# Kernel optimization log

Hardware: AMD Instinct MI355X
Metric: run time of the kernel (lower is better)

The kernel has to match this reference:

```python
import jax, jax.numpy as jnp
import numpy as np

B, T, C, H, M, MEM_FREQ = 1, 2048, 768, 12, 64, 64


def setup_inputs() -> dict:
    key = jax.random.key(0)
    k1, k2, k3 = jax.random.split(key, 3)
    x = jax.random.normal(k1, (B, T, C), jnp.float32)
    # landmark ('mem') token every MEM_FREQ positions, as in landmark-attention data prep
    is_mem = jnp.broadcast_to((jnp.arange(T) % MEM_FREQ == MEM_FREQ - 1)[None, :], (B, T))
    w_qkv = 0.02 * jax.random.normal(k2, (C, 3 * C), jnp.float32)
    b_qkv = jnp.zeros((3 * C,), jnp.float32)
    w_proj = 0.02 * jax.random.normal(k3, (C, C), jnp.float32)
    b_proj = jnp.zeros((C,), jnp.float32)
    return {"x": x, "is_mem": is_mem, "w_qkv": w_qkv, "b_qkv": b_qkv,
            "w_proj": w_proj, "b_proj": b_proj}


def _grouped_softmax(att, im, mask, last_sec):
    """LandmarkGroupedSoftmaxFunction + landmark_grouped_softmax (eval, no dropout).
    att/im/mask/last_sec: (B,H,T,T); softmax over last dim grouped into M buckets."""
    neg = -jnp.inf
    last_and_rest = last_sec | mask
    full_access = im | last_and_rest
    mem_group_idx = jnp.cumsum(im.astype(jnp.int32), axis=-1)  # (B,H,T,T)
    resp = jnp.where(last_and_rest | im, M - 1, mem_group_idx)  # bucket id per key

    R = att.shape[0] * att.shape[1] * att.shape[2]
    Tk = att.shape[3]
    xf = att.reshape(R, Tk)
    idxf = resp.reshape(R, Tk)

    row_max = jax.vmap(lambda xr, ir: jnp.full((M,), neg, xr.dtype).at[ir].max(xr))
    row_sum = jax.vmap(lambda xr, ir: jnp.zeros((M,), xr.dtype).at[ir].add(xr))

    max_by_group = row_max(xf, idxf)                                   # (R,M)
    maxes = jnp.take_along_axis(max_by_group, idxf, axis=-1)
    safe_max = jnp.where(jnp.isinf(maxes), 0.0, maxes)
    x_exp = jnp.exp(xf - safe_max)
    denom_g = row_sum(x_exp, idxf)
    denom = jnp.take_along_axis(denom_g, idxf, axis=-1)
    small = denom < 0.5
    probs = jnp.where(small, 0.0, x_exp / jnp.where(small, 1.0, denom))

    imf = im.reshape(R, Tk)
    lsf = last_sec.reshape(R, Tk)
    faf = full_access.reshape(R, Tk)
    # group_prob[g] = prob of landmark g; last slot = mass of last (current) section
    gp_idx = jnp.where(imf, mem_group_idx.reshape(R, Tk) - 1, M - 1)
    group_prob = row_sum(jnp.where(imf, probs, 0.0), gp_idx)
    group_prob = group_prob.at[:, M - 1].set(jnp.sum(probs * lsf, axis=-1))
    gathered = jnp.take_along_axis(group_prob, idxf, axis=-1)
    mult = jnp.where(faf, lsf.astype(probs.dtype), gathered)
    return (probs * mult).reshape(att.shape)


def reference(x, is_mem, w_qkv, b_qkv, w_proj, b_proj):
    Bx, Tx, Cx = x.shape
    hd = Cx // H
    qkv = x @ w_qkv + b_qkv
    q, k, v = jnp.split(qkv, 3, axis=-1)
    q = q.reshape(Bx, Tx, H, hd).transpose(0, 2, 1, 3)  # (B,H,T,hd)
    k = k.reshape(Bx, Tx, H, hd).transpose(0, 2, 1, 3)
    v = v.reshape(Bx, Tx, H, hd).transpose(0, 2, 1, 3)

    att = jnp.einsum('bhqd,bhkd->bhqk', q, k) * (1.0 / np.sqrt(hd))
    causal = jnp.triu(jnp.ones((Tx, Tx), bool), 1)[None, None]  # True = masked
    att = jnp.where(causal, -jnp.inf, att)

    im = jnp.broadcast_to(is_mem[:, None, None, :], (Bx, H, Tx, Tx))
    im_i = im.astype(jnp.int32)
    mem_ids = jnp.where(causal, 0, jnp.cumsum(im_i, axis=-1) - im_i)
    last_sec = mem_ids == jnp.max(mem_ids, axis=-1, keepdims=True)
    mask = causal | (im & last_sec)   # landmarks of the current section are masked
    last_sec = last_sec & ~mask
    im = im & ~mask
    att = jnp.where(mask, -jnp.inf, att)

    probs = _grouped_softmax(att, im, mask, last_sec)
    y = jnp.einsum('bhqk,bhkd->bhqd', probs, v)
    y = y.transpose(0, 2, 1, 3).reshape(Bx, Tx, Cx)
    return y @ w_proj + b_proj
```

## Files before the change

### kernel.cpp

```cpp
#include <hip/hip_runtime.h>
#include <hip/hip_bf16.h>
#include <math.h>

#define TT 2048
#define CC 768
#define NH 12
#define HDIM 64
#define QKVLD 2304
#define NSEC 32
#define NCH 8
#define NCHMAX 4
#define NSLOTS 960

typedef short bf16x8 __attribute__((ext_vector_type(8)));
typedef float f32x4 __attribute__((ext_vector_type(4)));

#define MFMA16(a, b, c) __builtin_amdgcn_mfma_f32_16x16x32_bf16(a, b, c, 0, 0, 0)

__device__ __forceinline__ ushort f2bf(float f) {
  __hip_bfloat16 h = __float2bfloat16(f);
  return *reinterpret_cast<ushort*>(&h);
}

__device__ __forceinline__ float bf2f(ushort u) {
  __hip_bfloat16 b = *reinterpret_cast<__hip_bfloat16*>(&u);
  return __bfloat162float(b);
}

__device__ __forceinline__ void gload_lds16(const ushort* g, ushort* l) {
  __builtin_amdgcn_global_load_lds(
      (const __attribute__((address_space(1))) void*)g,
      (__attribute__((address_space(3))) void*)l, 16, 0, 0);
}

__device__ __forceinline__ int chunk_base(int q) {
  const int a = q >> 3, b = q & 7;
  return q + 4 * a * (a - 1) + a * b;
}

__global__ __launch_bounds__(256) void prep_kernel(
    const float* __restrict__ x, const float* __restrict__ w_qkv,
    const float* __restrict__ w_proj,
    ushort* __restrict__ xb, ushort* __restrict__ wqkvT,
    ushort* __restrict__ wprojT) {
  const int bid = blockIdx.x;
  const int t = threadIdx.x;
  __shared__ float tile[64][65];

  if (bid < 768) {
    const int i = (bid * 256 + t) * 8;
    float4 a = *(const float4*)&x[i];
    float4 b = *(const float4*)&x[i + 4];
    bf16x8 o;
    o[0] = (short)f2bf(a.x); o[1] = (short)f2bf(a.y);
    o[2] = (short)f2bf(a.z); o[3] = (short)f2bf(a.w);
    o[4] = (short)f2bf(b.x); o[5] = (short)f2bf(b.y);
    o[6] = (short)f2bf(b.z); o[7] = (short)f2bf(b.w);
    *(bf16x8*)&xb[i] = o;
    return;
  }

  const bool qkv = bid < 1200;
  const int tb = qkv ? bid - 768 : bid - 1200;
  const float* in = qkv ? w_qkv : w_proj;
  ushort* out = qkv ? wqkvT : wprojT;
  const int N = qkv ? QKVLD : CC;
  const int ntx = N / 64;
  const int nb = (tb % ntx) * 64, kb = (tb / ntx) * 64;
  const int K = CC;

  const int rg = t >> 4, cg = t & 15;
#pragma unroll
  for (int r = 0; r < 4; ++r) {
    float4 v = *(const float4*)&in[(size_t)(kb + rg * 4 + r) * N + nb + cg * 4];
    tile[rg * 4 + r][cg * 4 + 0] = v.x;
    tile[rg * 4 + r][cg * 4 + 1] = v.y;
    tile[rg * 4 + r][cg * 4 + 2] = v.z;
    tile[rg * 4 + r][cg * 4 + 3] = v.w;
  }
  __syncthreads();
#pragma unroll
  for (int r = 0; r < 4; ++r) {
    const int nl = rg * 4 + r;
    ushort4 o;
    o.x = f2bf(tile[cg * 4 + 0][nl]);
    o.y = f2bf(tile[cg * 4 + 1][nl]);
    o.z = f2bf(tile[cg * 4 + 2][nl]);
    o.w = f2bf(tile[cg * 4 + 3][nl]);
    *(ushort4*)&out[(size_t)(nb + nl) * K + kb + cg * 4] = o;
  }
}

__global__ __launch_bounds__(256) void gemm_bt_bf16_kernel(
    const ushort* __restrict__ A, const ushort* __restrict__ Bt,
    const float* __restrict__ bias,
    ushort* __restrict__ qkvb, ushort* __restrict__ vT,
    float* __restrict__ Cf,
    int M, int N, int K) {
  __shared__ ushort As[2][64 * 64];
  __shared__ ushort Bs[2][64 * 64];
  const int tid = threadIdx.x;
  const int wid = tid >> 6, lane = tid & 63;
  const int lr = lane & 15, lg = lane >> 4;
  const int wr = wid >> 1, wc = wid & 1;
  const int bm = blockIdx.y * 64, bn = blockIdx.x * 64;

  f32x4 acc[2][2];
#pragma unroll
  for (int m = 0; m < 2; ++m)
#pragma unroll
    for (int n = 0; n < 2; ++n) acc[m][n] = (f32x4){0.f, 0.f, 0.f, 0.f};

  const int srow7 = lane >> 3;
  const int scolw = ((lane & 7) ^ srow7) * 8;
  const int rswz = lr & 7;

#pragma unroll
  for (int half = 0; half < 2; ++half) {
    const int row = half * 32 + wid * 8 + srow7;
    gload_lds16(A  + (size_t)(bm + row) * K + scolw, &As[0][(half * 32 + wid * 8) * 64]);
    gload_lds16(Bt + (size_t)(bn + row) * K + scolw, &Bs[0][(half * 32 + wid * 8) * 64]);
  }
  int cur = 0;

  for (int k0 = 0; k0 < K; k0 += 64) {
    __syncthreads();
    if (k0 + 64 < K) {
      const int nb_ = cur ^ 1;
#pragma unroll
      for (int half = 0; half < 2; ++half) {
        const int row = half * 32 + wid * 8 + srow7;
        gload_lds16(A  + (size_t)(bm + row) * K + k0 + 64 + scolw,
                    &As[nb_][(half * 32 + wid * 8) * 64]);
        gload_lds16(Bt + (size_t)(bn + row) * K + k0 + 64 + scolw,
                    &Bs[nb_][(half * 32 + wid * 8) * 64]);
      }
    }
#pragma unroll
    for (int kk = 0; kk < 2; ++kk) {
      bf16x8 af[2], bfr[2];
#pragma unroll
      for (int m = 0; m < 2; ++m)
        af[m] = *(const bf16x8*)
            &As[cur][(wr * 32 + m * 16 + lr) * 64 + (((kk * 4 + lg) ^ rswz) * 8)];
#pragma unroll
      for (int n = 0; n < 2; ++n)
        bfr[n] = *(const bf16x8*)
            &Bs[cur][(wc * 32 + n * 16 + lr) * 64 + (((kk * 4 + lg) ^ rswz) * 8)];
#pragma unroll
      for (int m = 0; m < 2; ++m)
#pragma unroll
        for (int n = 0; n < 2; ++n)
          acc[m][n] = MFMA16(af[m], bfr[n], acc[m][n]);
    }
    cur ^= 1;
  }

  float bb[2];
#pragma unroll
  for (int n = 0; n < 2; ++n) bb[n] = bias[bn + wc * 32 + n * 16 + lr];

  if (Cf) {
#pragma unroll
    for (int m = 0; m < 2; ++m)
#pragma unroll
      for (int n = 0; n < 2; ++n)
#pragma unroll
        for (int r = 0; r < 4; ++r) {
          const int row = bm + wr * 32 + m * 16 + lg * 4 + r;
          const int col = bn + wc * 32 + n * 16 + lr;
          Cf[(size_t)row * N + col] = acc[m][n][r] + bb[n];
        }
  } else if (bn < 768) {
#pragma unroll
    for (int m = 0; m < 2; ++m)
#pragma unroll
      for (int n = 0; n < 2; ++n)
#pragma unroll
        for (int r = 0; r < 4; ++r) {
          const int row = bm + wr * 32 + m * 16 + lg * 4 + r;
          const int col = bn + wc * 32 + n * 16 + lr;
          qkvb[(size_t)row * QKVLD + col] = f2bf((acc[m][n][r] + bb[n]) * 0.125f);
        }
  } else if (bn < 1536) {
#pragma unroll
    for (int m = 0; m < 2; ++m)
#pragma unroll
      for (int n = 0; n < 2; ++n)
#pragma unroll
        for (int r = 0; r < 4; ++r) {
          const int row = bm + wr * 32 + m * 16 + lg * 4 + r;
          const int col = bn + wc * 32 + n * 16 + lr;
          qkvb[(size_t)row * QKVLD + col] = f2bf(acc[m][n][r] + bb[n]);
        }
  } else {
#pragma unroll
    for (int m = 0; m < 2; ++m)
#pragma unroll
      for (int n = 0; n < 2; ++n) {
        const int row0 = bm + wr * 32 + m * 16 + lg * 4;
        const int vrow = bn + wc * 32 + n * 16 + lr - 1536;
        ushort4 o;
        o.x = f2bf(acc[m][n][0] + bb[n]);
        o.y = f2bf(acc[m][n][1] + bb[n]);
        o.z = f2bf(acc[m][n][2] + bb[n]);
        o.w = f2bf(acc[m][n][3] + bb[n]);
        *(ushort4*)&vT[(size_t)vrow * TT + row0] = o;
      }
  }
}

__global__ __launch_bounds__(256, 4) void attn_chunk_kernel(
    const ushort* __restrict__ qkvb,
    const ushort* __restrict__ vT,
    ushort* __restrict__ pacc,
    float* __restrict__ pstats) {
  const int c = blockIdx.x, qsec = blockIdx.y, h = blockIdx.z;
  if (c * NCH > qsec) return;
  const int tid = threadIdx.x;
  const int wid = tid >> 6, lane = tid & 63;
  const int lr = lane & 15, lg = lane >> 4;

  __shared__ ushort Kl[2][64 * 64];
  __shared__ ushort Vl[2][64 * 64];
  __shared__ ushort Pl[4 * 16 * 64];

  const int qloc = wid * 16 + lr;
  const ushort* qp = qkvb + (size_t)(qsec * 64 + qloc) * QKVLD + h * HDIM + lg * 8;
  const bf16x8 qf0 = *(const bf16x8*)qp;
  const bf16x8 qf1 = *(const bf16x8*)(qp + 32);

  f32x4 accy[4];
#pragma unroll
  for (int nt = 0; nt < 4; ++nt) accy[nt] = (f32x4){0.f, 0.f, 0.f, 0.f};
  float mrun = -INFINITY, dl = 0.f;

  const int s0 = c * NCH;
  const int send = (s0 + NCH - 1 < qsec) ? s0 + NCH - 1 : qsec;

  const int srow = wid * 8 + (lane >> 3);
  const int scolw = ((lane & 7) ^ (lane >> 3)) * 8;
  const ushort* ksrc = qkvb + (size_t)(s0 * 64 + srow) * QKVLD + CC + h * HDIM + scolw;
  const ushort* vsrc = vT + (size_t)(h * HDIM + srow) * TT + s0 * 64 + scolw;
  const int rswz = lr & 7;

  gload_lds16(ksrc,                      &Kl[0][wid * 512]);
  gload_lds16(ksrc + (size_t)32 * QKVLD, &Kl[0][wid * 512 + 2048]);
  gload_lds16(vsrc,                      &Vl[0][wid * 512]);
  gload_lds16(vsrc + (size_t)32 * TT,    &Vl[0][wid * 512 + 2048]);
  int cur = 0;

  for (int s = s0; s <= send; ++s) {
    __syncthreads();
    if (s < send) {
      ksrc += (size_t)64 * QKVLD;
      vsrc += 64;
      const int nb_ = cur ^ 1;
      gload_lds16(ksrc,                      &Kl[nb_][wid * 512]);
      gload_lds16(ksrc + (size_t)32 * QKVLD, &Kl[nb_][wid * 512 + 2048]);
      gload_lds16(vsrc,                      &Vl[nb_][wid * 512]);
      gload_lds16(vsrc + (size_t)32 * TT,    &Vl[nb_][wid * 512 + 2048]);
    }

    f32x4 sacc[4];
#pragma unroll
    for (int nt = 0; nt < 4; ++nt) sacc[nt] = (f32x4){0.f, 0.f, 0.f, 0.f};
#pragma unroll
    for (int nt = 0; nt < 4; ++nt) {
      bf16x8 kf0 = *(const bf16x8*)&Kl[cur][(nt * 16 + lr) * 64 + ((lg ^ rswz) * 8)];
      bf16x8 kf1 = *(const bf16x8*)&Kl[cur][(nt * 16 + lr) * 64 + (((4 + lg) ^ rswz) * 8)];
      sacc[nt] = MFMA16(kf0, qf0, sacc[nt]);
      sacc[nt] = MFMA16(kf1, qf1, sacc[nt]);
    }

    const bool curq = (s == qsec);
    float lmv = 0.f;
    if (!curq) {
      lmv = __shfl(sacc[3][3], 48 + lr);
      if (lg == 3) sacc[3][3] = -INFINITY;
    } else {
      const int lim = qloc < 62 ? qloc : 62;
#pragma unroll
      for (int nt = 0; nt < 4; ++nt)
#pragma unroll
        for (int r = 0; r < 4; ++r)
          if (nt * 16 + lg * 4 + r > lim) sacc[nt][r] = -INFINITY;
    }

    float vmax = sacc[0][0];
#pragma unroll
    for (int nt = 0; nt < 4; ++nt)
#pragma unroll
      for (int r = 0; r < 4; ++r) vmax = fmaxf(vmax, sacc[nt][r]);
    vmax = fmaxf(vmax, __shfl_xor(vmax, 16));
    vmax = fmaxf(vmax, __shfl_xor(vmax, 32));

    float base_;
    if (curq) {
      float mn = fmaxf(mrun, vmax);
      float sc = __expf(mrun - mn);
#pragma unroll
      for (int nt = 0; nt < 4; ++nt) accy[nt] *= sc;
      dl *= sc; mrun = mn; base_ = mn;
    } else {
      base_ = vmax;
    }

    float ssum = 0.f;
#pragma unroll
    for (int nt = 0; nt < 4; ++nt)
#pragma unroll
      for (int r = 0; r < 4; ++r) {
        sacc[nt][r] = __expf(sacc[nt][r] - base_);
        ssum += sacc[nt][r];
      }
    ssum += __shfl_xor(ssum, 16);
    ssum += __shfl_xor(ssum, 32);

    float coef;
    if (!curq) {
      float mn = fmaxf(mrun, lmv);
      float sc = __expf(mrun - mn);
      float el = __expf(lmv - mn);
#pragma unroll
      for (int nt = 0; nt < 4; ++nt) accy[nt] *= sc;
      dl = dl * sc + el; mrun = mn;
      coef = el / ssum;
    } else {
      coef = 1.f;
      dl += ssum;
    }

    {
      ushort* prow = &Pl[wid * 1024 + lr * 64];
#pragma unroll
      for (int nt = 0; nt < 4; ++nt) {
        ushort4 o;
        o.x = f2bf(sacc[nt][0] * coef);
        o.y = f2bf(sacc[nt][1] * coef);
        o.z = f2bf(sacc[nt][2] * coef);
        o.w = f2bf(sacc[nt][3] * coef);
        *(ushort4*)&prow[(((nt * 2 + (lg >> 1)) ^ rswz) * 8) + (lg & 1) * 4] = o;
      }

      bf16x8 pf0 = *(const bf16x8*)&prow[(lg ^ rswz) * 8];
      bf16x8 pf1 = *(const bf16x8*)&prow[((4 + lg) ^ rswz) * 8];
#pragma unroll
      for (int nt = 0; nt < 4; ++nt) {
        bf16x8 vf0 = *(const bf16x8*)&Vl[cur][(nt * 16 + lr) * 64 + ((lg ^ rswz) * 8)];
        bf16x8 vf1 = *(const bf16x8*)&Vl[cur][(nt * 16 + lr) * 64 + (((4 + lg) ^ rswz) * 8)];
        accy[nt] = MFMA16(vf0, pf0, accy[nt]);
        accy[nt] = MFMA16(vf1, pf1, accy[nt]);
      }
    }
    cur ^= 1;
  }

  const int slot = (chunk_base(qsec) + c) * NH + h;
  ushort* ap = pacc + (size_t)slot * 4096;
#pragma unroll
  for (int nt = 0; nt < 4; ++nt)
#pragma unroll
    for (int r = 0; r < 4; ++r)
      ap[(nt * 16 + lg * 4 + r) * 64 + wid * 16 + lr] = f2bf(accy[nt][r]);
  if (lg == 0) {
    float* st = pstats + (size_t)slot * 128;
    st[(wid * 16 + lr) * 2 + 0] = mrun;
    st[(wid * 16 + lr) * 2 + 1] = dl;
  }
}

__global__ __launch_bounds__(256) void attn_merge_kernel(
    const ushort* __restrict__ pacc, const float* __restrict__ pstats,
    ushort* __restrict__ y) {
  const int qsec = blockIdx.x, h = blockIdx.y;
  const int tid = threadIdx.x;
  const int w = tid >> 6, q = tid & 63;
  const int nch = (qsec >> 3) + 1;
  const int sbase = chunk_base(qsec);
  __shared__ float Lt[64][65];

  float M = -INFINITY;
  for (int cc = 0; cc < nch; ++cc)
    M = fmaxf(M, pstats[(size_t)((sbase + cc) * NH + h) * 128 + q * 2]);
  float D = 0.f;
  for (int cc = 0; cc < nch; ++cc) {
    const float* st = pstats + (size_t)((sbase + cc) * NH + h) * 128 + q * 2;
    D += __expf(st[0] - M) * st[1];
  }
  const float invD = 1.f / D;

  float val[16];
#pragma unroll
  for (int j = 0; j < 16; ++j) val[j] = 0.f;
  for (int cc = 0; cc < nch; ++cc) {
    const int slot = (sbase + cc) * NH + h;
    const float cw = __expf(pstats[(size_t)slot * 128 + q * 2] - M) * invD;
    const ushort* ap = pacc + (size_t)slot * 4096 + w * 16 * 64 + q;
#pragma unroll
    for (int j = 0; j < 16; ++j) val[j] += cw * bf2f(ap[j * 64]);
  }
#pragma unroll
  for (int j = 0; j < 16; ++j) Lt[w * 16 + j][q] = val[j];
  __syncthreads();

  const int d = tid & 63;
#pragma unroll
  for (int j = 0; j < 16; ++j) {
    const int qq = w * 16 + j;
    y[(size_t)(qsec * 64 + qq) * CC + h * HDIM + d] = f2bf(Lt[d][qq]);
  }
}

extern "C" void kernel_launch(void* const* d_in, const int* in_sizes, int n_in,
                              void* d_out, int out_size, void* d_ws, size_t ws_size,
                              hipStream_t stream) {
  const float* x      = (const float*)d_in[0];
  const float* w_qkv  = (const float*)d_in[2];
  const float* b_qkv  = (const float*)d_in[3];
  const float* w_proj = (const float*)d_in[4];
  const float* b_proj = (const float*)d_in[5];
  float* out = (float*)d_out;

  ushort* wprojT = (ushort*)d_ws;
  ushort* qkvb   = wprojT + (size_t)CC * CC;
  ushort* vT     = qkvb + (size_t)TT * QKVLD;
  ushort* y      = vT + (size_t)CC * TT;
  ushort* pacc   = y + (size_t)TT * CC;
  float*  pstats = (float*)(pacc + (size_t)NSLOTS * 4096);
  ushort* xb     = pacc;
  ushort* wqkvT  = xb + (size_t)TT * CC;

  prep_kernel<<<1344, 256, 0, stream>>>(x, w_qkv, w_proj, xb, wqkvT, wprojT);

  gemm_bt_bf16_kernel<<<dim3(QKVLD / 64, TT / 64), 256, 0, stream>>>(
      xb, wqkvT, b_qkv, qkvb, vT, nullptr, TT, QKVLD, CC);

  attn_chunk_kernel<<<dim3(NCHMAX, NSEC, NH), 256, 0, stream>>>(
      qkvb, vT, pacc, pstats);
  attn_merge_kernel<<<dim3(NSEC, NH), 256, 0, stream>>>(pacc, pstats, y);

  gemm_bt_bf16_kernel<<<dim3(CC / 64, TT / 64), 256, 0, stream>>>(
      y, wprojT, b_proj, nullptr, nullptr, out, TT, CC, CC);
}
```

Measured before the change: 76.79 us.

## Replace double-buffered direct-to-LDS loads with register-staged single-buffer prefetch

The attention chunk kernel drops its double-buffered K/V shared-memory tiles fed by global-to-LDS loads. It now prefetches the next tile into registers, writes it to a single LDS buffer between two barriers, and raises the launch-bounds occupancy hint from 4 to 6 blocks. The aim is to cut LDS use and so fit more resident blocks per CU. The cost is an extra barrier per iteration, extra VGPRs for staging, and explicit LDS stores replacing the direct loads.

```diff
diff --git a/kernel.cpp b/kernel.cpp
--- a/kernel.cpp
+++ b/kernel.cpp
@@ -210,7 +210,7 @@
   }
 }
 
-__global__ __launch_bounds__(256, 4) void attn_chunk_kernel(
+__global__ __launch_bounds__(256, 6) void attn_chunk_kernel(
     const ushort* __restrict__ qkvb,
     const ushort* __restrict__ vT,
     ushort* __restrict__ pacc,
@@ -221,8 +221,8 @@
   const int wid = tid >> 6, lane = tid & 63;
   const int lr = lane & 15, lg = lane >> 4;
 
-  __shared__ ushort Kl[2][64 * 64];
-  __shared__ ushort Vl[2][64 * 64];
+  __shared__ ushort Kl[64 * 64];
+  __shared__ ushort Vl[64 * 64];
   __shared__ ushort Pl[4 * 16 * 64];
 
   const int qloc = wid * 16 + lr;
@@ -240,26 +240,30 @@
 
   const int srow = wid * 8 + (lane >> 3);
   const int scolw = ((lane & 7) ^ (lane >> 3)) * 8;
+  const int dstoff = wid * 512 + lane * 8;
   const ushort* ksrc = qkvb + (size_t)(s0 * 64 + srow) * QKVLD + CC + h * HDIM + scolw;
   const ushort* vsrc = vT + (size_t)(h * HDIM + srow) * TT + s0 * 64 + scolw;
   const int rswz = lr & 7;
 
-  gload_lds16(ksrc,                      &Kl[0][wid * 512]);
-  gload_lds16(ksrc + (size_t)32 * QKVLD, &Kl[0][wid * 512 + 2048]);
-  gload_lds16(vsrc,                      &Vl[0][wid * 512]);
-  gload_lds16(vsrc + (size_t)32 * TT,    &Vl[0][wid * 512 + 2048]);
-  int cur = 0;
+  bf16x8 kr0 = *(const bf16x8*)ksrc;
+  bf16x8 kr1 = *(const bf16x8*)(ksrc + (size_t)32 * QKVLD);
+  bf16x8 vr0 = *(const bf16x8*)vsrc;
+  bf16x8 vr1 = *(const bf16x8*)(vsrc + (size_t)32 * TT);
 
   for (int s = s0; s <= send; ++s) {
+    __syncthreads();
+    *(bf16x8*)&Kl[dstoff]        = kr0;
+    *(bf16x8*)&Kl[dstoff + 2048] = kr1;
+    *(bf16x8*)&Vl[dstoff]        = vr0;
+    *(bf16x8*)&Vl[dstoff + 2048] = vr1;
     __syncthreads();
     if (s < send) {
       ksrc += (size_t)64 * QKVLD;
       vsrc += 64;
-      const int nb_ = cur ^ 1;
-      gload_lds16(ksrc,                      &Kl[nb_][wid * 512]);
-      gload_lds16(ksrc + (size_t)32 * QKVLD, &Kl[nb_][wid * 512 + 2048]);
-      gload_lds16(vsrc,                      &Vl[nb_][wid * 512]);
-      gload_lds16(vsrc + (size_t)32 * TT,    &Vl[nb_][wid * 512 + 2048]);
+      kr0 = *(const bf16x8*)ksrc;
+      kr1 = *(const bf16x8*)(ksrc + (size_t)32 * QKVLD);
+      vr0 = *(const bf16x8*)vsrc;
+      vr1 = *(const bf16x8*)(vsrc + (size_t)32 * TT);
     }
 
     f32x4 sacc[4];
@@ -267,8 +271,8 @@
     for (int nt = 0; nt < 4; ++nt) sacc[nt] = (f32x4){0.f, 0.f, 0.f, 0.f};
 #pragma unroll
     for (int nt = 0; nt < 4; ++nt) {
-      bf16x8 kf0 = *(const bf16x8*)&Kl[cur][(nt * 16 + lr) * 64 + ((lg ^ rswz) * 8)];
-      bf16x8 kf1 = *(const bf16x8*)&Kl[cur][(nt * 16 + lr) * 64 + (((4 + lg) ^ rswz) * 8)];
+      bf16x8 kf0 = *(const bf16x8*)&Kl[(nt * 16 + lr) * 64 + ((lg ^ rswz) * 8)];
+      bf16x8 kf1 = *(const bf16x8*)&Kl[(nt * 16 + lr) * 64 + (((4 + lg) ^ rswz) * 8)];
       sacc[nt] = MFMA16(kf0, qf0, sacc[nt]);
       sacc[nt] = MFMA16(kf1, qf1, sacc[nt]);
     }
@@ -347,13 +351,12 @@
       bf16x8 pf1 = *(const bf16x8*)&prow[((4 + lg) ^ rswz) * 8];
 #pragma unroll
       for (int nt = 0; nt < 4; ++nt) {
-        bf16x8 vf0 = *(const bf16x8*)&Vl[cur][(nt * 16 + lr) * 64 + ((lg ^ rswz) * 8)];
-        bf16x8 vf1 = *(const bf16x8*)&Vl[cur][(nt * 16 + lr) * 64 + (((4 + lg) ^ rswz) * 8)];
+        bf16x8 vf0 = *(const bf16x8*)&Vl[(nt * 16 + lr) * 64 + ((lg ^ rswz) * 8)];
+        bf16x8 vf1 = *(const bf16x8*)&Vl[(nt * 16 + lr) * 64 + (((4 + lg) ^ rswz) * 8)];
         accy[nt] = MFMA16(vf0, pf0, accy[nt]);
         accy[nt] = MFMA16(vf1, pf1, accy[nt]);
       }
     }
-    cur ^= 1;
   }
 
   const int slot = (chunk_base(qsec) + c) * NH + h;
```

Result: slower. 122.3 us (+59.3%).
